# Optimization experiments

Hardware: AMD Instinct MI355X
Metric: run time of the kernel (lower is better)

The kernel has to match this reference:

```python
import jax, jax.numpy as jnp
import numpy as np

N_NODES = 100000


def gcn_conv(x, edge_index, weight, num_nodes):
    """PyG GCNConv (bias=False): transform -> add self-loops -> sym-normalized scatter-add."""
    h = x @ weight  # [N, out]
    src, dst = edge_index[0], edge_index[1]
    loop = jnp.arange(num_nodes, dtype=src.dtype)
    src = jnp.concatenate([src, loop])
    dst = jnp.concatenate([dst, loop])
    ones = jnp.ones(src.shape[0], dtype=h.dtype)
    deg = jax.ops.segment_sum(ones, dst, num_segments=num_nodes)  # in-degree incl. self-loop
    dis = jnp.where(deg > 0, jax.lax.rsqrt(deg), 0.0)             # deg^-1/2, inf -> 0
    norm = dis[src] * dis[dst]                                    # [E+N]
    msg = norm[:, None] * h[src]                                  # gather + scale
    return jax.ops.segment_sum(msg, dst, num_segments=num_nodes)  # scatter-add


def setup_inputs() -> dict:
    key = jax.random.key(0)
    k1, k2, k3, k4 = jax.random.split(key, 4)
    x = jax.random.normal(k1, (N_NODES, 512), dtype=jnp.float32)
    edge_index = jax.random.randint(k2, (2, 3200000), 0, N_NODES, dtype=jnp.int64)
    weight1 = jax.random.normal(k3, (512, 16), dtype=jnp.float32) * 0.05
    weight2 = jax.random.normal(k4, (16, 16), dtype=jnp.float32) * 0.25
    return {"x": x, "edge_index": edge_index, "weight1": weight1, "weight2": weight2}


def reference(x, edge_index, weight1, weight2):
    n = x.shape[0]
    h = gcn_conv(x, edge_index, weight1, n)
    out = gcn_conv(h, edge_index, weight2, n)
    return out
```

## Files before the change

kernel.cpp:

```cpp
#include <hip/hip_runtime.h>
#include <hip/hip_bf16.h>


#define N_NODES 100000
#define F_IN 512
#define F_OUT 16
#define WS_PAD 516

__global__ __launch_bounds__(256) void k_gemm1(const float* __restrict__ x,
                                               const float* __restrict__ W,
                                               float* __restrict__ h, int nrows) {
    __shared__ __align__(16) float Ws[F_OUT * WS_PAD];
    for (int i = threadIdx.x; i < F_IN * F_OUT; i += 256) {
        int k = i >> 4, o = i & 15;
        Ws[o * WS_PAD + k] = W[i];
    }
    __syncthreads();

    int l = threadIdx.x & 15;
    int r = blockIdx.x * 16 + (threadIdx.x >> 4);
    if (r >= nrows) return;

    const float4* xr = (const float4*)(x + (size_t)r * F_IN);
    float4 v[8];
#pragma unroll
    for (int c = 0; c < 8; ++c) v[c] = xr[c * 16 + l];

    const float* wrow = Ws + l * WS_PAD;
    float acc = 0.0f;
#pragma unroll
    for (int c = 0; c < 8; ++c) {
#pragma unroll
        for (int t = 0; t < 16; ++t) {
            float4 wv = *(const float4*)(wrow + c * 64 + t * 4);
            float ax = __shfl(v[c].x, t, 16);
            float ay = __shfl(v[c].y, t, 16);
            float az = __shfl(v[c].z, t, 16);
            float aw = __shfl(v[c].w, t, 16);
            acc = fmaf(ax, wv.x, acc);
            acc = fmaf(ay, wv.y, acc);
            acc = fmaf(az, wv.z, acc);
            acc = fmaf(aw, wv.w, acc);
        }
    }
    h[(size_t)r * 16 + l] = acc;
}

__global__ __launch_bounds__(256) void k_gemm2(const float* __restrict__ a,
                                               const float* __restrict__ W,
                                               float* __restrict__ h2, int nrows) {
    __shared__ float Ws[F_OUT * 17];
    if (threadIdx.x < 256) {
        int i = threadIdx.x;
        int k = i >> 4, o = i & 15;
        Ws[o * 17 + k] = W[i];
    }
    __syncthreads();
    int l = threadIdx.x & 15;
    int r = blockIdx.x * 16 + (threadIdx.x >> 4);
    if (r >= nrows) return;
    float av = a[(size_t)r * 16 + l];
    const float* wrow = Ws + l * 17;
    float acc = 0.0f;
#pragma unroll
    for (int t = 0; t < 16; ++t) {
        float xv = __shfl(av, t, 16);
        acc = fmaf(xv, wrow[t], acc);
    }
    h2[(size_t)r * 16 + l] = acc;
}

__global__ void k_zero_i32(int* __restrict__ p, int n) {
    int i = blockIdx.x * blockDim.x + threadIdx.x;
    if (i < n) p[i] = 0;
}

__global__ void k_hist(const int* __restrict__ dst, int* __restrict__ deg, int E) {
    int e = blockIdx.x * blockDim.x + threadIdx.x;
    if (e < E) atomicAdd(&deg[dst[e]], 1);
}

__global__ void k_dis(const int* __restrict__ deg, float* __restrict__ dis, int n) {
    int i = blockIdx.x * blockDim.x + threadIdx.x;
    if (i < n) dis[i] = rsqrtf(1.0f + (float)deg[i]);
}

__global__ __launch_bounds__(256) void k_scan1(const int* __restrict__ deg,
                                               int* __restrict__ rowp,
                                               int* __restrict__ bsum, int n) {
    __shared__ int s[256];
    int i = threadIdx.x;
    int gi = blockIdx.x * 256 + i;
    int v = (gi < n) ? deg[gi] : 0;
    s[i] = v;
    __syncthreads();
#pragma unroll
    for (int off = 1; off < 256; off <<= 1) {
        int t = (i >= off) ? s[i - off] : 0;
        __syncthreads();
        s[i] += t;
        __syncthreads();
    }
    if (gi < n) rowp[gi] = s[i] - v;
    if (i == 255) bsum[blockIdx.x] = s[255];
}

__global__ __launch_bounds__(512) void k_scan2(int* __restrict__ bsum, int nb) {
    __shared__ int s[512];
    int i = threadIdx.x;
    int v = (i < nb) ? bsum[i] : 0;
    s[i] = v;
    __syncthreads();
#pragma unroll
    for (int off = 1; off < 512; off <<= 1) {
        int t = (i >= off) ? s[i - off] : 0;
        __syncthreads();
        s[i] += t;
        __syncthreads();
    }
    if (i < nb) bsum[i] = s[i] - v;
}

__global__ void k_scan3(int* __restrict__ rowp, int* __restrict__ pos,
                        const int* __restrict__ bsum, int n, int E) {
    int gi = blockIdx.x * blockDim.x + threadIdx.x;
    if (gi < n) {
        int r = rowp[gi] + bsum[blockIdx.x * blockDim.x / 256 + (threadIdx.x >= 0 ? 0 : 0)];
        r = rowp[gi] + bsum[gi >> 8];
        rowp[gi] = r;
        pos[gi] = r;
    }
    if (gi == 0) rowp[n] = E;
}

__global__ void k_fill(const int* __restrict__ src, const int* __restrict__ dst,
                       int* __restrict__ pos, int* __restrict__ esrc, int E) {
    int e = blockIdx.x * blockDim.x + threadIdx.x;
    if (e < E) {
        int d = dst[e];
        int slot = atomicAdd(&pos[d], 1);
        esrc[slot] = src[e];
    }
}

__global__ __launch_bounds__(256) void k_agg(const int* __restrict__ rowp,
                                             const int* __restrict__ esrc,
                                             const float* __restrict__ dis,
                                             const float* __restrict__ h,
                                             float* __restrict__ out, int n) {
    int tid = blockIdx.x * 256 + threadIdx.x;
    int node = tid >> 4;
    int c = tid & 15;
    if (node >= n) return;
    float dd = dis[node];
    float acc = dd * dd * h[(size_t)node * 16 + c];
    int b = rowp[node], e = rowp[node + 1];
    for (int j = b; j < e; ++j) {
        int s = esrc[j];
        float w = dd * dis[s];
        acc = fmaf(w, h[(size_t)s * 16 + c], acc);
    }
    out[(size_t)node * 16 + c] = acc;
}

__global__ void k_deg_init(float* __restrict__ deg, int n) {
    int i = blockIdx.x * blockDim.x + threadIdx.x;
    if (i < n) deg[i] = 1.0f;
}
__global__ void k_deg_count(const int* __restrict__ dst, float* __restrict__ deg, int E) {
    int e = blockIdx.x * blockDim.x + threadIdx.x;
    if (e < E) unsafeAtomicAdd(&deg[dst[e]], 1.0f);
}
__global__ void k_rsqrt(float* __restrict__ deg, int n) {
    int i = blockIdx.x * blockDim.x + threadIdx.x;
    if (i < n) deg[i] = rsqrtf(deg[i]);
}
__global__ void k_selfloop_init(const float* __restrict__ dis, const float* __restrict__ h,
                                float* __restrict__ out, int total) {
    int t = blockIdx.x * blockDim.x + threadIdx.x;
    if (t >= total) return;
    int i = t >> 4;
    float d = dis[i];
    out[t] = d * d * h[t];
}
__global__ __launch_bounds__(256) void k_scatter(const int* __restrict__ src,
                                                 const int* __restrict__ dst,
                                                 const float* __restrict__ dis,
                                                 const float* __restrict__ h,
                                                 float* __restrict__ out, int E) {
    int gid = blockIdx.x * 256 + threadIdx.x;
    int e = gid >> 4;
    if (e >= E) return;
    int c = gid & 15;
    int s = src[e];
    int d = dst[e];
    float v = dis[s] * dis[d] * h[(size_t)s * 16 + c];
    unsafeAtomicAdd(&out[(size_t)d * 16 + c], v);
}

extern "C" void kernel_launch(void* const* d_in, const int* in_sizes, int n_in,
                              void* d_out, int out_size, void* d_ws, size_t ws_size,
                              hipStream_t stream) {
    const float* x  = (const float*)d_in[0];
    const int*   ei = (const int*)d_in[1];
    const float* W1 = (const float*)d_in[2];
    const float* W2 = (const float*)d_in[3];
    float* out = (float*)d_out;

    const int N = N_NODES;
    const int E = in_sizes[1] / 2;
    const int* src = ei;
    const int* dst = ei + E;
    const int B = 256;
    const int nb = (N + 255) / 256;

    float* dis  = (float*)d_ws;
    float* bufA = dis + N;
    float* bufB = bufA + (size_t)N * 16;
    int* deg  = (int*)(bufB + (size_t)N * 16);
    int* rowp = deg + N;
    int* pos  = rowp + (N + 1);
    int* bsum = pos + N;
    int* esrc = bsum + 512;
    size_t needed = (size_t)((char*)(esrc + E) - (char*)d_ws);

    if (ws_size >= needed) {
        k_zero_i32<<<(N + B - 1) / B, B, 0, stream>>>(deg, N);
        k_hist<<<(E + B - 1) / B, B, 0, stream>>>(dst, deg, E);
        k_dis<<<(N + B - 1) / B, B, 0, stream>>>(deg, dis, N);
        k_scan1<<<nb, 256, 0, stream>>>(deg, rowp, bsum, N);
        k_scan2<<<1, 512, 0, stream>>>(bsum, nb);
        k_scan3<<<nb, 256, 0, stream>>>(rowp, pos, bsum, N, E);
        k_fill<<<(E + B - 1) / B, B, 0, stream>>>(src, dst, pos, esrc, E);

        k_gemm1<<<(N + 15) / 16, B, 0, stream>>>(x, W1, bufA, N);
        k_agg<<<(N * 16 + B - 1) / B, B, 0, stream>>>(rowp, esrc, dis, bufA, bufB, N);
        k_gemm2<<<(N + 15) / 16, B, 0, stream>>>(bufB, W2, bufA, N);
        k_agg<<<(N * 16 + B - 1) / B, B, 0, stream>>>(rowp, esrc, dis, bufA, out, N);
    } else {
        float* fdis = (float*)d_ws;
        float* h1   = fdis + N;
        float* out1 = h1 + (size_t)N * 16;
        float* h2   = out1 + (size_t)N * 16;
        const int NC = N * F_OUT;

        k_deg_init<<<(N + B - 1) / B, B, 0, stream>>>(fdis, N);
        k_deg_count<<<(E + B - 1) / B, B, 0, stream>>>(dst, fdis, E);
        k_rsqrt<<<(N + B - 1) / B, B, 0, stream>>>(fdis, N);

        k_gemm1<<<(N + 15) / 16, B, 0, stream>>>(x, W1, h1, N);
        k_selfloop_init<<<(NC + B - 1) / B, B, 0, stream>>>(fdis, h1, out1, NC);
        {
            long long threads = (long long)E * 16;
            k_scatter<<<(unsigned)((threads + B - 1) / B), B, 0, stream>>>(src, dst, fdis, h1, out1, E);
        }
        k_gemm2<<<(N + 15) / 16, B, 0, stream>>>(out1, W2, h2, N);
        k_selfloop_init<<<(NC + B - 1) / B, B, 0, stream>>>(fdis, h2, out, NC);
        {
            long long threads = (long long)E * 16;
            k_scatter<<<(unsigned)((threads + B - 1) / B), B, 0, stream>>>(src, dst, fdis, h2, out, E);
        }
    }
}
```

Measured before the change: 980.4 us.

## Replace CSR build with coarse destination-bucket partition and shared-memory aggregation

Drops the per-node CSR construction (three-pass scan plus a per-edge global atomic fill). Edges are instead partitioned into 512 buckets of 196 destination nodes, staged through per-block shared-memory queues, and stored as packed src/local-dst words. Aggregation runs one block per bucket and accumulates messages with shared-memory float atomics before a single coalesced write that also folds in the self-loop. The aim is to cut the random global atomics and the load imbalance between nodes of different degree. In exchange it adds contention on the shared-memory atomics, gives no ordering within a bucket, and relies on node ids fitting in 17 bits.

Measured after the change: 1.285 ms. 1.31x slower.

```diff
diff --git a/kernel.cpp b/kernel.cpp
--- a/kernel.cpp
+++ b/kernel.cpp
@@ -5,7 +5,134 @@
 #define N_NODES 100000
 #define F_IN 512
 #define F_OUT 16
+#define NB 512
+#define RNG 196
+#define QCAP 24
 #define WS_PAD 516
+
+__global__ void k_zero_i32(int* __restrict__ p, int n) {
+    int i = blockIdx.x * blockDim.x + threadIdx.x;
+    if (i < n) p[i] = 0;
+}
+
+__global__ void k_hist(const int* __restrict__ dst, int* __restrict__ deg, int E) {
+    int e = blockIdx.x * blockDim.x + threadIdx.x;
+    if (e < E) atomicAdd(&deg[dst[e]], 1);
+}
+
+__global__ void k_dis(const int* __restrict__ deg, float* __restrict__ dis, int n) {
+    int i = blockIdx.x * blockDim.x + threadIdx.x;
+    if (i < n) dis[i] = rsqrtf(1.0f + (float)deg[i]);
+}
+
+__global__ void k_bucket_count(const int* __restrict__ deg, int* __restrict__ bcnt, int n) {
+    int b = blockIdx.x * blockDim.x + threadIdx.x;
+    if (b >= NB) return;
+    int beg = b * RNG, end = min(n, beg + RNG);
+    int sum = 0;
+    for (int i = beg; i < end; ++i) sum += deg[i];
+    bcnt[b] = (beg < n) ? sum : 0;
+}
+
+__global__ __launch_bounds__(512) void k_scan_buckets(const int* __restrict__ bcnt,
+                                                      int* __restrict__ bbase,
+                                                      int* __restrict__ cur) {
+    __shared__ int s[NB];
+    int i = threadIdx.x;
+    int v = bcnt[i];
+    s[i] = v;
+    __syncthreads();
+#pragma unroll
+    for (int off = 1; off < NB; off <<= 1) {
+        int t = (i >= off) ? s[i - off] : 0;
+        __syncthreads();
+        s[i] += t;
+        __syncthreads();
+    }
+    int excl = s[i] - v;
+    bbase[i] = excl;
+    cur[i] = excl;
+    if (i == NB - 1) bbase[NB] = s[NB - 1];
+}
+
+__global__ __launch_bounds__(256) void k_partition(const int* __restrict__ src,
+                                                   const int* __restrict__ dst,
+                                                   int* __restrict__ cur,
+                                                   unsigned* __restrict__ ebuf,
+                                                   int E, int per) {
+    __shared__ unsigned q[NB][QCAP];
+    __shared__ int qc[NB];
+    for (int i = threadIdx.x; i < NB; i += 256) qc[i] = 0;
+    __syncthreads();
+
+    int beg = blockIdx.x * per;
+    int end = min(E, beg + per);
+    for (int e = beg + threadIdx.x; e < end; e += 256) {
+        int s = src[e], d = dst[e];
+        int b = d / RNG;
+        unsigned ent = (unsigned)s | ((unsigned)(d - b * RNG) << 17);
+        int c = atomicAdd(&qc[b], 1);
+        if (c < QCAP) q[b][c] = ent;
+        else ebuf[atomicAdd(&cur[b], 1)] = ent;
+    }
+    __syncthreads();
+
+    int g = threadIdx.x >> 4, l = threadIdx.x & 15;
+    for (int b = g; b < NB; b += 16) {
+        int c = qc[b];
+        if (c > QCAP) c = QCAP;
+        if (c == 0) continue;
+        int base = 0;
+        if (l == 0) base = atomicAdd(&cur[b], c);
+        base = __shfl(base, 0, 16);
+        for (int i = l; i < c; i += 16) ebuf[base + i] = q[b][i];
+    }
+}
+
+__global__ __launch_bounds__(512) void k_agg_bucket(const unsigned* __restrict__ ebuf,
+                                                    const int* __restrict__ bbase,
+                                                    const float* __restrict__ dis,
+                                                    const float* __restrict__ h,
+                                                    float* __restrict__ out, int n) {
+    __shared__ float acc[RNG * 16];
+    for (int i = threadIdx.x; i < RNG * 16; i += 512) acc[i] = 0.0f;
+    __syncthreads();
+
+    int b = blockIdx.x;
+    int beg = bbase[b], end = bbase[b + 1];
+    int g = threadIdx.x >> 4, l = threadIdx.x & 15;
+
+    for (int idx = beg + g; idx < end; idx += 64) {
+        unsigned e0 = ebuf[idx];
+        int s0 = e0 & 0x1FFFF;
+        int d0 = e0 >> 17;
+        float w0 = dis[s0];
+        float h0 = h[(size_t)s0 * 16 + l];
+        int i1 = idx + 32;
+        if (i1 < end) {
+            unsigned e1 = ebuf[i1];
+            int s1 = e1 & 0x1FFFF;
+            int d1 = e1 >> 17;
+            float w1 = dis[s1];
+            float h1v = h[(size_t)s1 * 16 + l];
+            atomicAdd(&acc[d0 * 16 + l], w0 * h0);
+            atomicAdd(&acc[d1 * 16 + l], w1 * h1v);
+        } else {
+            atomicAdd(&acc[d0 * 16 + l], w0 * h0);
+        }
+    }
+    __syncthreads();
+
+    int base_node = b * RNG;
+    for (int nl = g; nl < RNG; nl += 32) {
+        int node = base_node + nl;
+        if (node < n) {
+            float dd = dis[node];
+            size_t o = (size_t)node * 16 + l;
+            out[o] = dd * (dd * h[o] + acc[nl * 16 + l]);
+        }
+    }
+}
 
 __global__ __launch_bounds__(256) void k_gemm1(const float* __restrict__ x,
                                                const float* __restrict__ W,
@@ -68,99 +195,6 @@
         acc = fmaf(xv, wrow[t], acc);
     }
     h2[(size_t)r * 16 + l] = acc;
-}
-
-__global__ void k_zero_i32(int* __restrict__ p, int n) {
-    int i = blockIdx.x * blockDim.x + threadIdx.x;
-    if (i < n) p[i] = 0;
-}
-
-__global__ void k_hist(const int* __restrict__ dst, int* __restrict__ deg, int E) {
-    int e = blockIdx.x * blockDim.x + threadIdx.x;
-    if (e < E) atomicAdd(&deg[dst[e]], 1);
-}
-
-__global__ void k_dis(const int* __restrict__ deg, float* __restrict__ dis, int n) {
-    int i = blockIdx.x * blockDim.x + threadIdx.x;
-    if (i < n) dis[i] = rsqrtf(1.0f + (float)deg[i]);
-}
-
-__global__ __launch_bounds__(256) void k_scan1(const int* __restrict__ deg,
-                                               int* __restrict__ rowp,
-                                               int* __restrict__ bsum, int n) {
-    __shared__ int s[256];
-    int i = threadIdx.x;
-    int gi = blockIdx.x * 256 + i;
-    int v = (gi < n) ? deg[gi] : 0;
-    s[i] = v;
-    __syncthreads();
-#pragma unroll
-    for (int off = 1; off < 256; off <<= 1) {
-        int t = (i >= off) ? s[i - off] : 0;
-        __syncthreads();
-        s[i] += t;
-        __syncthreads();
-    }
-    if (gi < n) rowp[gi] = s[i] - v;
-    if (i == 255) bsum[blockIdx.x] = s[255];
-}
-
-__global__ __launch_bounds__(512) void k_scan2(int* __restrict__ bsum, int nb) {
-    __shared__ int s[512];
-    int i = threadIdx.x;
-    int v = (i < nb) ? bsum[i] : 0;
-    s[i] = v;
-    __syncthreads();
-#pragma unroll
-    for (int off = 1; off < 512; off <<= 1) {
-        int t = (i >= off) ? s[i - off] : 0;
-        __syncthreads();
-        s[i] += t;
-        __syncthreads();
-    }
-    if (i < nb) bsum[i] = s[i] - v;
-}
-
-__global__ void k_scan3(int* __restrict__ rowp, int* __restrict__ pos,
-                        const int* __restrict__ bsum, int n, int E) {
-    int gi = blockIdx.x * blockDim.x + threadIdx.x;
-    if (gi < n) {
-        int r = rowp[gi] + bsum[blockIdx.x * blockDim.x / 256 + (threadIdx.x >= 0 ? 0 : 0)];
-        r = rowp[gi] + bsum[gi >> 8];
-        rowp[gi] = r;
-        pos[gi] = r;
-    }
-    if (gi == 0) rowp[n] = E;
-}
-
-__global__ void k_fill(const int* __restrict__ src, const int* __restrict__ dst,
-                       int* __restrict__ pos, int* __restrict__ esrc, int E) {
-    int e = blockIdx.x * blockDim.x + threadIdx.x;
-    if (e < E) {
-        int d = dst[e];
-        int slot = atomicAdd(&pos[d], 1);
-        esrc[slot] = src[e];
-    }
-}
-
-__global__ __launch_bounds__(256) void k_agg(const int* __restrict__ rowp,
-                                             const int* __restrict__ esrc,
-                                             const float* __restrict__ dis,
-                                             const float* __restrict__ h,
-                                             float* __restrict__ out, int n) {
-    int tid = blockIdx.x * 256 + threadIdx.x;
-    int node = tid >> 4;
-    int c = tid & 15;
-    if (node >= n) return;
-    float dd = dis[node];
-    float acc = dd * dd * h[(size_t)node * 16 + c];
-    int b = rowp[node], e = rowp[node + 1];
-    for (int j = b; j < e; ++j) {
-        int s = esrc[j];
-        float w = dd * dis[s];
-        acc = fmaf(w, h[(size_t)s * 16 + c], acc);
-    }
-    out[(size_t)node * 16 + c] = acc;
 }
 
 __global__ void k_deg_init(float* __restrict__ deg, int n) {
@@ -212,31 +246,31 @@
     const int* src = ei;
     const int* dst = ei + E;
     const int B = 256;
-    const int nb = (N + 255) / 256;
 
     float* dis  = (float*)d_ws;
     float* bufA = dis + N;
     float* bufB = bufA + (size_t)N * 16;
-    int* deg  = (int*)(bufB + (size_t)N * 16);
-    int* rowp = deg + N;
-    int* pos  = rowp + (N + 1);
-    int* bsum = pos + N;
-    int* esrc = bsum + 512;
-    size_t needed = (size_t)((char*)(esrc + E) - (char*)d_ws);
+    int* deg   = (int*)(bufB + (size_t)N * 16);
+    int* bcnt  = deg + N;
+    int* bbase = bcnt + NB;
+    int* cur   = bbase + NB + 1;
+    unsigned* ebuf = (unsigned*)(cur + NB);
+    size_t needed = (size_t)((char*)(ebuf + E) - (char*)d_ws);
 
     if (ws_size >= needed) {
         k_zero_i32<<<(N + B - 1) / B, B, 0, stream>>>(deg, N);
         k_hist<<<(E + B - 1) / B, B, 0, stream>>>(dst, deg, E);
         k_dis<<<(N + B - 1) / B, B, 0, stream>>>(deg, dis, N);
-        k_scan1<<<nb, 256, 0, stream>>>(deg, rowp, bsum, N);
-        k_scan2<<<1, 512, 0, stream>>>(bsum, nb);
-        k_scan3<<<nb, 256, 0, stream>>>(rowp, pos, bsum, N, E);
-        k_fill<<<(E + B - 1) / B, B, 0, stream>>>(src, dst, pos, esrc, E);
-
+        k_bucket_count<<<(NB + B - 1) / B, B, 0, stream>>>(deg, bcnt, N);
+        k_scan_buckets<<<1, NB, 0, stream>>>(bcnt, bbase, cur);
+        {
+            int per = (E + NB - 1) / NB;
+            k_partition<<<NB, 256, 0, stream>>>(src, dst, cur, ebuf, E, per);
+        }
         k_gemm1<<<(N + 15) / 16, B, 0, stream>>>(x, W1, bufA, N);
-        k_agg<<<(N * 16 + B - 1) / B, B, 0, stream>>>(rowp, esrc, dis, bufA, bufB, N);
+        k_agg_bucket<<<NB, 512, 0, stream>>>(ebuf, bbase, dis, bufA, bufB, N);
         k_gemm2<<<(N + 15) / 16, B, 0, stream>>>(bufB, W2, bufA, N);
-        k_agg<<<(N * 16 + B - 1) / B, B, 0, stream>>>(rowp, esrc, dis, bufA, out, N);
+        k_agg_bucket<<<NB, 512, 0, stream>>>(ebuf, bbase, dis, bufA, out, N);
     } else {
         float* fdis = (float*)d_ws;
         float* h1   = fdis + N;
```
